# Kernel optimization log

Measured on AMD Instinct MI355X. Metric: run time of the kernel, lower is better.

## Reference

```python
import jax, jax.numpy as jnp
import numpy as np

D_MODEL = 1024
H = 16
D_K = D_MODEL // H


def setup_inputs() -> dict:
    key = jax.random.key(0)
    ks = jax.random.split(key, 12)
    B, S = 2, 2048
    q = jax.random.normal(ks[0], (B, S, D_MODEL), dtype=jnp.float32)
    k = jax.random.normal(ks[1], (B, S, D_MODEL), dtype=jnp.float32)
    v = jax.random.normal(ks[2], (B, S, D_MODEL), dtype=jnp.float32)
    mask = jax.random.randint(ks[3], (1, 1, S, S), 0, 2, dtype=jnp.int32)
    sc = 1.0 / np.sqrt(D_MODEL)
    wq = jax.random.uniform(ks[4], (D_MODEL, D_MODEL), jnp.float32, -sc, sc)
    bq = jax.random.uniform(ks[5], (D_MODEL,), jnp.float32, -sc, sc)
    wk = jax.random.uniform(ks[6], (D_MODEL, D_MODEL), jnp.float32, -sc, sc)
    bk = jax.random.uniform(ks[7], (D_MODEL,), jnp.float32, -sc, sc)
    wv = jax.random.uniform(ks[8], (D_MODEL, D_MODEL), jnp.float32, -sc, sc)
    bv = jax.random.uniform(ks[9], (D_MODEL,), jnp.float32, -sc, sc)
    wo = jax.random.uniform(ks[10], (D_MODEL, D_MODEL), jnp.float32, -sc, sc)
    bo = jax.random.uniform(ks[11], (D_MODEL,), jnp.float32, -sc, sc)
    return {"q": q, "k": k, "v": v, "mask": mask,
            "wq": wq, "bq": bq, "wk": wk, "bk": bk,
            "wv": wv, "bv": bv, "wo": wo, "bo": bo}


def reference(q, k, v, mask, wq, bq, wk, bk, wv, bv, wo, bo):
    B, S, _ = q.shape
    # linear projections (torch Linear: x @ W.T + b)
    query = q @ wq.T + bq
    key = k @ wk.T + bk
    value = v @ wv.T + bv
    # [B, S, D] -> [B, H, S, d_k]
    query = query.reshape(B, S, H, D_K).transpose(0, 2, 1, 3)
    key = key.reshape(B, S, H, D_K).transpose(0, 2, 1, 3)
    value = value.reshape(B, S, H, D_K).transpose(0, 2, 1, 3)
    scores = jnp.einsum('bhqd,bhkd->bhqk', query, key) / jnp.sqrt(
        jnp.asarray(D_K, query.dtype))
    # NOTE: source uses `-1 ** 9` which is -1 in Python, not -1e9 (soft mask)
    scores = jnp.where(mask == 0, jnp.asarray(-1.0, scores.dtype), scores)
    attn = jax.nn.softmax(scores, axis=-1)
    # source calls dropout(attn) but discards the result -> no-op
    x = jnp.einsum('bhqk,bhkd->bhqd', attn, value)
    x = x.transpose(0, 2, 1, 3).reshape(B, S, H * D_K)
    return x @ wo.T + bo
```

## Files before the change

kernel.cpp:

```cpp
#include <hip/hip_runtime.h>
#include <hip/hip_bf16.h>

#define D_MODEL 1024
#define NH 16
#define DK 64
#define S_LEN 2048
#define BATCH 2
#define M_ROWS (BATCH * S_LEN)

typedef float    floatx4 __attribute__((ext_vector_type(4)));
typedef _Float16 half8   __attribute__((ext_vector_type(8)));
typedef _Float16 half4v  __attribute__((ext_vector_type(4)));

#define LOG2E 1.4426950408889634f
#define EXPM1 0.36787944117144233f

__device__ __forceinline__ half8 ldh8(const _Float16* p) {
    return __builtin_bit_cast(half8, *(const uint4*)p);
}
__device__ __forceinline__ void gld16(const void* g, void* l) {
    __builtin_amdgcn_global_load_lds(
        (const __attribute__((address_space(1))) void*)g,
        (__attribute__((address_space(3))) void*)l, 16, 0, 0);
}
__device__ __forceinline__ float dpp_swap1(float x) {
    return __builtin_bit_cast(float,
        __builtin_amdgcn_mov_dpp(__builtin_bit_cast(int, x), 0xB1, 0xF, 0xF, false));
}

__global__ __launch_bounds__(256)
void cast_h(const float* __restrict__ s0, const float* __restrict__ s1,
            const float* __restrict__ s2, const float* __restrict__ s3,
            _Float16* __restrict__ out, int R) {
    const int z = blockIdx.y;
    const float* src = (z == 0) ? s0 : (z == 1) ? s1 : (z == 2) ? s2 : s3;
    const size_t idx = ((size_t)blockIdx.x * 256 + threadIdx.x) * 4;
    float4 v = *(const float4*)&src[idx];
    half4v h = {(_Float16)v.x, (_Float16)v.y, (_Float16)v.z, (_Float16)v.w};
    *(half4v*)&out[(size_t)z * R * 1024 + idx] = h;
}

template <int OUTMODE>
__global__ __launch_bounds__(256)
void gemm_f16(const _Float16* __restrict__ Abase, const _Float16* __restrict__ Wbase,
              const float* __restrict__ b0, const float* __restrict__ b1,
              const float* __restrict__ b2, void* __restrict__ Obase) {
    __shared__ __align__(16) _Float16 As[128 * 64];
    __shared__ __align__(16) _Float16 Ws[128 * 64];
    const int tid = threadIdx.x;
    const int w = tid >> 6, lane = tid & 63;
    const int l15 = lane & 15, q4 = lane >> 4;
    const int z = (OUTMODE == 1) ? blockIdx.z : 0;
    const int m0 = blockIdx.y * 128, n0 = blockIdx.x * 128;
    const int wm = w >> 1, wn = w & 1;

    const _Float16* A = Abase + (size_t)z * M_ROWS * 1024;
    const _Float16* W = Wbase + (size_t)z * 1024 * 1024;
    const float* bias = (OUTMODE == 1) ? ((z == 0) ? b0 : (z == 1) ? b1 : b2) : b0;

    int srow[4], sseg[4];
#pragma unroll
    for (int i = 0; i < 4; i++) {
        const int slot = i * 256 + tid;
        srow[i] = slot >> 3;
        sseg[i] = ((slot & 7) ^ (srow[i] & 7)) * 8;
    }

    int aoff[4][2], woff[4][2];
#pragma unroll
    for (int r = 0; r < 4; r++) {
        const int ar = wm * 64 + r * 16 + l15;
        const int wr = wn * 64 + r * 16 + l15;
#pragma unroll
        for (int kc = 0; kc < 2; kc++) {
            aoff[r][kc] = (ar * 8 + ((kc * 4 + q4) ^ (ar & 7))) * 8;
            woff[r][kc] = (wr * 8 + ((kc * 4 + q4) ^ (wr & 7))) * 8;
        }
    }

    floatx4 acc[4][4];
#pragma unroll
    for (int r = 0; r < 4; r++)
#pragma unroll
        for (int c = 0; c < 4; c++) acc[r][c] = (floatx4){0.f, 0.f, 0.f, 0.f};

    for (int k0 = 0; k0 < 1024; k0 += 64) {
#pragma unroll
        for (int i = 0; i < 4; i++) {
            const int lb = (i * 256 + w * 64) * 8;
            gld16(&A[(size_t)(m0 + srow[i]) * 1024 + k0 + sseg[i]], &As[lb]);
            gld16(&W[(size_t)(n0 + srow[i]) * 1024 + k0 + sseg[i]], &Ws[lb]);
        }
        __syncthreads();

        half8 af[4][2], wf[4][2];
#pragma unroll
        for (int r = 0; r < 4; r++)
#pragma unroll
            for (int kc = 0; kc < 2; kc++) {
                af[r][kc] = ldh8(&As[aoff[r][kc]]);
                wf[r][kc] = ldh8(&Ws[woff[r][kc]]);
            }
#pragma unroll
        for (int kc = 0; kc < 2; kc++)
#pragma unroll
            for (int r = 0; r < 4; r++)
#pragma unroll
                for (int c = 0; c < 4; c++)
                    acc[r][c] = __builtin_amdgcn_mfma_f32_16x16x32_f16(
                        af[r][kc], wf[c][kc], acc[r][c], 0, 0, 0);
        __syncthreads();
    }

#pragma unroll
    for (int r = 0; r < 4; r++)
#pragma unroll
        for (int c = 0; c < 4; c++)
#pragma unroll
            for (int reg = 0; reg < 4; reg++) {
                const int m = m0 + wm * 64 + r * 16 + q4 * 4 + reg;
                const int n = n0 + wn * 64 + c * 16 + l15;
                float val = acc[r][c][reg] + bias[n];
                if (OUTMODE == 0) {
                    ((float*)Obase)[(size_t)m * 1024 + n] = val;
                } else {
                    if (z == 0) val *= 0.125f * LOG2E;
                    const int b = m >> 11, s = m & 2047;
                    const int h = n >> 6, d = n & 63;
                    _Float16* Oz = (_Float16*)Obase + (size_t)z * M_ROWS * 1024;
                    Oz[(((size_t)(b * 16 + h) * S_LEN + s) << 6) + d] = (_Float16)val;
                }
            }
}

__global__ __launch_bounds__(256)
void vt_trans(const short* __restrict__ Vh, short* __restrict__ Vt) {
    __shared__ __align__(16) short T[64][80];
    const int bh = blockIdx.y;
    const int s0 = blockIdx.x * 64;
    const int t = threadIdx.x;
#pragma unroll
    for (int i = 0; i < 2; i++) {
        const int p = t + i * 256, r = p >> 3, c8 = (p & 7) * 8;
        uint4 raw = *(const uint4*)&Vh[((size_t)bh * S_LEN + s0 + r) * 64 + c8];
        const short* sv = (const short*)&raw;
#pragma unroll
        for (int j = 0; j < 8; j++) T[c8 + j][r] = sv[j];
    }
    __syncthreads();
#pragma unroll
    for (int i = 0; i < 2; i++) {
        const int p = t + i * 256, d = p >> 3, seg = (p & 7) * 8;
        *(uint4*)&Vt[((size_t)bh * DK + d) * S_LEN + s0 + seg] =
            *(const uint4*)&T[d][seg];
    }
}

__global__ __launch_bounds__(256)
void mask_pack(const int* __restrict__ mask, unsigned long long* __restrict__ mb) {
    const int gw = blockIdx.x * 4 + (threadIdx.x >> 6);
    const int lane = threadIdx.x & 63;
    const int row = gw >> 5, wid = gw & 31;
    const int mv = mask[(size_t)row * S_LEN + wid * 64 + lane];
    unsigned long long bal = __ballot(mv != 0);
    if (lane == 0) mb[gw] = bal;
}

__global__ __launch_bounds__(512, 4)
void attn_mfma(const _Float16* __restrict__ Qh, const _Float16* __restrict__ Kh,
               const _Float16* __restrict__ Vt, const unsigned long long* __restrict__ mb,
               _Float16* __restrict__ Xh) {
    __shared__ __align__(16) _Float16 Ks[2][64 * 64];
    __shared__ __align__(16) _Float16 Vs[2][64 * 64];
    __shared__ __align__(16) _Float16 Ps[8][32 * 72];

    const int tid = threadIdx.x;
    const int w = tid >> 6, lane = tid & 63;
    const int z = w >> 2, w4 = w & 3;
    const int t255 = tid & 255;
    const int l15 = lane & 15, q4 = lane >> 4;
    const int bh = blockIdx.y, b = bh >> 4, h = bh & 15;
    const int qb = blockIdx.x * 128 + w4 * 32;
    const int kbase = z * 1024;

    const _Float16* Qg = Qh + ((size_t)bh * S_LEN + qb) * DK;
    const _Float16* Kg = Kh + ((size_t)bh * S_LEN + kbase) * DK;
    const _Float16* Vg = Vt + (size_t)bh * DK * S_LEN + kbase;

    half8 Aq[2][2];
#pragma unroll
    for (int qs = 0; qs < 2; qs++)
#pragma unroll
        for (int ch = 0; ch < 2; ch++)
            Aq[qs][ch] = ldh8(&Qg[(qs * 16 + l15) * DK + ch * 32 + q4 * 8]);

    int grow[2], gseg[2];
#pragma unroll
    for (int i = 0; i < 2; i++) {
        const int slot = i * 256 + t255;
        grow[i] = slot >> 3;
        gseg[i] = ((slot & 7) ^ (grow[i] & 7)) * 8;
    }

    int kb[2];
#pragma unroll
    for (int ch = 0; ch < 2; ch++)
        kb[ch] = l15 * 64 + (((ch * 4 + q4) ^ (l15 & 7)) * 8);

    const unsigned long long* mrow_p = mb + (size_t)(qb + q4 * 4) * (S_LEN / 64) + z * 16;

    floatx4 O[2][4];
#pragma unroll
    for (int qs = 0; qs < 2; qs++)
#pragma unroll
        for (int nt = 0; nt < 4; nt++) O[qs][nt] = (floatx4){0.f, 0.f, 0.f, 0.f};
    floatx4 lacc[2];
    lacc[0] = (floatx4){0.f, 0.f, 0.f, 0.f};
    lacc[1] = (floatx4){0.f, 0.f, 0.f, 0.f};

    half8 onesB;
#pragma unroll
    for (int i = 0; i < 8; i++) onesB[i] = (_Float16)1.0f;

    const bool evenlane = ((lane & 1) == 0);

    for (int j0 = 0; j0 < 1024; j0 += 64) {
#pragma unroll
        for (int i = 0; i < 2; i++) {
            const int lb = (i * 256 + w4 * 64) * 8;
            gld16(&Kg[(size_t)(j0 + grow[i]) * DK + gseg[i]], &Ks[z][lb]);
            gld16(&Vg[(size_t)grow[i] * S_LEN + j0 + gseg[i]], &Vs[z][lb]);
        }
        const int jw = j0 >> 6;
        __syncthreads();

#pragma unroll
        for (int qs = 0; qs < 2; qs++) {
            unsigned long long mw[4];
#pragma unroll
            for (int reg = 0; reg < 4; reg++)
                mw[reg] = mrow_p[qs * 512 + reg * 32 + jw];

            floatx4 Sf[4];
#pragma unroll
            for (int jt = 0; jt < 4; jt++) {
                floatx4 c = (floatx4){0.f, 0.f, 0.f, 0.f};
                c = __builtin_amdgcn_mfma_f32_16x16x32_f16(
                    Aq[qs][0], ldh8(&Ks[z][jt * 1024 + kb[0]]), c, 0, 0, 0);
                c = __builtin_amdgcn_mfma_f32_16x16x32_f16(
                    Aq[qs][1], ldh8(&Ks[z][jt * 1024 + kb[1]]), c, 0, 0, 0);
                Sf[jt] = c;
            }
#pragma unroll
            for (int reg = 0; reg < 4; reg++) {
                const unsigned long long m = mw[reg];
                const unsigned tt0 = (unsigned)m >> l15;
                const unsigned tt1 = (unsigned)(m >> 32) >> l15;
#pragma unroll
                for (int jt = 0; jt < 4; jt++) {
                    float p = __builtin_amdgcn_exp2f(Sf[jt][reg]);
                    const unsigned sel = (jt < 2 ? tt0 : tt1) & (1u << ((jt & 1) * 16));
                    p = sel ? p : EXPM1;
                    const float po = dpp_swap1(p);
                    if (evenlane) {
                        *(unsigned*)&Ps[w][(qs * 16 + q4 * 4 + reg) * 72 +
                                           jt * 16 + l15] =
                            __builtin_bit_cast(unsigned,
                                __builtin_amdgcn_cvt_pkrtz(p, po));
                    }
                }
            }
        }

#pragma unroll
        for (int qs = 0; qs < 2; qs++) {
            half8 Ap[2];
#pragma unroll
            for (int ch = 0; ch < 2; ch++)
                Ap[ch] = ldh8(&Ps[w][(qs * 16 + l15) * 72 + ch * 32 + q4 * 8]);
            lacc[qs] = __builtin_amdgcn_mfma_f32_16x16x32_f16(Ap[0], onesB, lacc[qs], 0, 0, 0);
            lacc[qs] = __builtin_amdgcn_mfma_f32_16x16x32_f16(Ap[1], onesB, lacc[qs], 0, 0, 0);
#pragma unroll
            for (int nt = 0; nt < 4; nt++) {
                O[qs][nt] = __builtin_amdgcn_mfma_f32_16x16x32_f16(
                    Ap[0], ldh8(&Vs[z][nt * 1024 + kb[0]]), O[qs][nt], 0, 0, 0);
                O[qs][nt] = __builtin_amdgcn_mfma_f32_16x16x32_f16(
                    Ap[1], ldh8(&Vs[z][nt * 1024 + kb[1]]), O[qs][nt], 0, 0, 0);
            }
        }
        __syncthreads();
    }

    float* Obuf = (float*)&Ps[0][0];
    if (z == 1) {
#pragma unroll
        for (int qs = 0; qs < 2; qs++)
#pragma unroll
            for (int reg = 0; reg < 4; reg++) {
                const int rl = w4 * 32 + qs * 16 + q4 * 4 + reg;
#pragma unroll
                for (int nt = 0; nt < 4; nt++)
                    Obuf[rl * 65 + nt * 16 + l15] = O[qs][nt][reg];
                if (l15 == 0) Obuf[rl * 65 + 64] = lacc[qs][reg];
            }
    }
    __syncthreads();
    if (z == 0) {
#pragma unroll
        for (int qs = 0; qs < 2; qs++)
#pragma unroll
            for (int reg = 0; reg < 4; reg++) {
                const int rl = w4 * 32 + qs * 16 + q4 * 4 + reg;
                const float inv = 1.0f / (lacc[qs][reg] + Obuf[rl * 65 + 64]);
                const int srow = qb + qs * 16 + q4 * 4 + reg;
                _Float16* Xrow = Xh + (size_t)(b * S_LEN + srow) * 1024 + h * DK;
#pragma unroll
                for (int nt = 0; nt < 4; nt++)
                    Xrow[nt * 16 + l15] =
                        (_Float16)((O[qs][nt][reg] + Obuf[rl * 65 + nt * 16 + l15]) * inv);
            }
    }
}

extern "C" void kernel_launch(void* const* d_in, const int* in_sizes, int n_in,
                              void* d_out, int out_size, void* d_ws, size_t ws_size,
                              hipStream_t stream) {
    const float* q  = (const float*)d_in[0];
    const float* k  = (const float*)d_in[1];
    const float* v  = (const float*)d_in[2];
    const int* mask = (const int*)d_in[3];
    const float* wq = (const float*)d_in[4];
    const float* bq = (const float*)d_in[5];
    const float* wk = (const float*)d_in[6];
    const float* bk = (const float*)d_in[7];
    const float* wv = (const float*)d_in[8];
    const float* bv = (const float*)d_in[9];
    const float* wo = (const float*)d_in[10];
    const float* bo = (const float*)d_in[11];
    float* out = (float*)d_out;

    char* ws = (char*)d_ws;
    const size_t MB = 1u << 20;
    _Float16* Wh   = (_Float16*)ws;
    _Float16* Ah   = (_Float16*)(ws + 8 * MB);
    _Float16* QKVh = (_Float16*)(ws + 32 * MB);
    _Float16* Vt   = (_Float16*)(ws + 56 * MB);
    unsigned long long* mb = (unsigned long long*)(ws + 64 * MB);
    _Float16* Xh   = Ah;

    cast_h<<<dim3(1024, 4), 256, 0, stream>>>(wq, wk, wv, wo, Wh, 1024);
    cast_h<<<dim3(4096, 3), 256, 0, stream>>>(q, k, v, nullptr, Ah, M_ROWS);

    gemm_f16<1><<<dim3(8, 32, 3), 256, 0, stream>>>(Ah, Wh, bq, bk, bv, QKVh);

    vt_trans<<<dim3(32, 32), 256, 0, stream>>>(
        (const short*)(QKVh + (size_t)2 * M_ROWS * 1024), (short*)Vt);
    mask_pack<<<S_LEN * (S_LEN / 64) / 4, 256, 0, stream>>>(mask, mb);

    attn_mfma<<<dim3(16, 32), 512, 0, stream>>>(QKVh, QKVh + (size_t)M_ROWS * 1024,
                                                Vt, mb, Xh);

    gemm_f16<0><<<dim3(8, 32, 1), 256, 0, stream>>>(Xh, Wh + (size_t)3 * 1024 * 1024,
                                                    bo, bo, bo, out);
}
```

Before: 285.8 us.

## Fuse V transpose into QKV GEMM epilogue and software-pipeline K/V loads in attention

The QKV projection GEMM now writes V directly in transposed [b,h,d,s] layout, which removes the separate vt_trans kernel launch and its read/write pass over V. In the attention kernel, K and V tile loads for the next iteration are issued right after the current tile is consumed. Explicit vmcnt waits and raw barriers replace the full __syncthreads, so the loads overlap with the QK and PV MFMA phases. Mask word loads are interleaved with the score MFMAs. The manual waitcnt and barrier choreography is fragile, and the loop issues one extra prefetch that wraps to index 0 on its last iteration.

```diff
diff --git a/kernel.cpp b/kernel.cpp
--- a/kernel.cpp
+++ b/kernel.cpp
@@ -26,6 +26,11 @@
 __device__ __forceinline__ float dpp_swap1(float x) {
     return __builtin_bit_cast(float,
         __builtin_amdgcn_mov_dpp(__builtin_bit_cast(int, x), 0xB1, 0xF, 0xF, false));
+}
+__device__ __forceinline__ void rawbar() {
+    __builtin_amdgcn_sched_barrier(0);
+    __builtin_amdgcn_s_barrier();
+    __builtin_amdgcn_sched_barrier(0);
 }
 
 __global__ __launch_bounds__(256)
@@ -44,7 +49,8 @@
 __global__ __launch_bounds__(256)
 void gemm_f16(const _Float16* __restrict__ Abase, const _Float16* __restrict__ Wbase,
               const float* __restrict__ b0, const float* __restrict__ b1,
-              const float* __restrict__ b2, void* __restrict__ Obase) {
+              const float* __restrict__ b2, void* __restrict__ Obase,
+              void* __restrict__ Obase2) {
     __shared__ __align__(16) _Float16 As[128 * 64];
     __shared__ __align__(16) _Float16 Ws[128 * 64];
     const int tid = threadIdx.x;
@@ -115,15 +121,29 @@
 #pragma unroll
     for (int r = 0; r < 4; r++)
 #pragma unroll
-        for (int c = 0; c < 4; c++)
-#pragma unroll
-            for (int reg = 0; reg < 4; reg++) {
-                const int m = m0 + wm * 64 + r * 16 + q4 * 4 + reg;
-                const int n = n0 + wn * 64 + c * 16 + l15;
-                float val = acc[r][c][reg] + bias[n];
-                if (OUTMODE == 0) {
-                    ((float*)Obase)[(size_t)m * 1024 + n] = val;
-                } else {
+        for (int c = 0; c < 4; c++) {
+            const int n = n0 + wn * 64 + c * 16 + l15;
+            const int mbase = m0 + wm * 64 + r * 16 + q4 * 4;
+            float vals[4];
+#pragma unroll
+            for (int reg = 0; reg < 4; reg++) vals[reg] = acc[r][c][reg] + bias[n];
+
+            if (OUTMODE == 0) {
+#pragma unroll
+                for (int reg = 0; reg < 4; reg++)
+                    ((float*)Obase)[(size_t)(mbase + reg) * 1024 + n] = vals[reg];
+            } else if (z == 2) {
+                const int b = mbase >> 11, s = mbase & 2047;
+                const int h = n >> 6, d = n & 63;
+                half4v hv = {(_Float16)vals[0], (_Float16)vals[1],
+                             (_Float16)vals[2], (_Float16)vals[3]};
+                *(half4v*)&((_Float16*)Obase2)[
+                    (((size_t)((b * 16 + h) * 64 + d)) << 11) + s] = hv;
+            } else {
+#pragma unroll
+                for (int reg = 0; reg < 4; reg++) {
+                    const int m = mbase + reg;
+                    float val = vals[reg];
                     if (z == 0) val *= 0.125f * LOG2E;
                     const int b = m >> 11, s = m & 2047;
                     const int h = n >> 6, d = n & 63;
@@ -131,29 +151,7 @@
                     Oz[(((size_t)(b * 16 + h) * S_LEN + s) << 6) + d] = (_Float16)val;
                 }
             }
-}
-
-__global__ __launch_bounds__(256)
-void vt_trans(const short* __restrict__ Vh, short* __restrict__ Vt) {
-    __shared__ __align__(16) short T[64][80];
-    const int bh = blockIdx.y;
-    const int s0 = blockIdx.x * 64;
-    const int t = threadIdx.x;
-#pragma unroll
-    for (int i = 0; i < 2; i++) {
-        const int p = t + i * 256, r = p >> 3, c8 = (p & 7) * 8;
-        uint4 raw = *(const uint4*)&Vh[((size_t)bh * S_LEN + s0 + r) * 64 + c8];
-        const short* sv = (const short*)&raw;
-#pragma unroll
-        for (int j = 0; j < 8; j++) T[c8 + j][r] = sv[j];
-    }
-    __syncthreads();
-#pragma unroll
-    for (int i = 0; i < 2; i++) {
-        const int p = t + i * 256, d = p >> 3, seg = (p & 7) * 8;
-        *(uint4*)&Vt[((size_t)bh * DK + d) * S_LEN + s0 + seg] =
-            *(const uint4*)&T[d][seg];
-    }
+        }
 }
 
 __global__ __launch_bounds__(256)
@@ -224,24 +222,28 @@
 
     const bool evenlane = ((lane & 1) == 0);
 
+#pragma unroll
+    for (int i = 0; i < 2; i++) {
+        const int lb = (i * 256 + w4 * 64) * 8;
+        gld16(&Kg[(size_t)grow[i] * DK + gseg[i]], &Ks[z][lb]);
+    }
+#pragma unroll
+    for (int i = 0; i < 2; i++) {
+        const int lb = (i * 256 + w4 * 64) * 8;
+        gld16(&Vg[(size_t)grow[i] * S_LEN + gseg[i]], &Vs[z][lb]);
+    }
+
     for (int j0 = 0; j0 < 1024; j0 += 64) {
-#pragma unroll
-        for (int i = 0; i < 2; i++) {
-            const int lb = (i * 256 + w4 * 64) * 8;
-            gld16(&Kg[(size_t)(j0 + grow[i]) * DK + gseg[i]], &Ks[z][lb]);
-            gld16(&Vg[(size_t)grow[i] * S_LEN + j0 + gseg[i]], &Vs[z][lb]);
-        }
+        const int jn = (j0 + 64) & 1023;
         const int jw = j0 >> 6;
-        __syncthreads();
+
+        __builtin_amdgcn_sched_barrier(0);
+        asm volatile("s_waitcnt vmcnt(2)" ::: "memory");
+        rawbar();
 
 #pragma unroll
         for (int qs = 0; qs < 2; qs++) {
             unsigned long long mw[4];
-#pragma unroll
-            for (int reg = 0; reg < 4; reg++)
-                mw[reg] = mrow_p[qs * 512 + reg * 32 + jw];
-
-            floatx4 Sf[4];
 #pragma unroll
             for (int jt = 0; jt < 4; jt++) {
                 floatx4 c = (floatx4){0.f, 0.f, 0.f, 0.f};
@@ -249,17 +251,17 @@
                     Aq[qs][0], ldh8(&Ks[z][jt * 1024 + kb[0]]), c, 0, 0, 0);
                 c = __builtin_amdgcn_mfma_f32_16x16x32_f16(
                     Aq[qs][1], ldh8(&Ks[z][jt * 1024 + kb[1]]), c, 0, 0, 0);
-                Sf[jt] = c;
-            }
-#pragma unroll
-            for (int reg = 0; reg < 4; reg++) {
-                const unsigned long long m = mw[reg];
-                const unsigned tt0 = (unsigned)m >> l15;
-                const unsigned tt1 = (unsigned)(m >> 32) >> l15;
-#pragma unroll
-                for (int jt = 0; jt < 4; jt++) {
-                    float p = __builtin_amdgcn_exp2f(Sf[jt][reg]);
-                    const unsigned sel = (jt < 2 ? tt0 : tt1) & (1u << ((jt & 1) * 16));
+                if (jt == 0) {
+#pragma unroll
+                    for (int reg = 0; reg < 4; reg++)
+                        mw[reg] = mrow_p[qs * 512 + reg * 32 + jw];
+                }
+#pragma unroll
+                for (int reg = 0; reg < 4; reg++) {
+                    const unsigned ttw =
+                        (unsigned)(mw[reg] >> (jt >= 2 ? 32 : 0)) >> l15;
+                    const unsigned sel = ttw & (1u << ((jt & 1) * 16));
+                    float p = __builtin_amdgcn_exp2f(c[reg]);
                     p = sel ? p : EXPM1;
                     const float po = dpp_swap1(p);
                     if (evenlane) {
@@ -272,6 +274,17 @@
             }
         }
 
+        rawbar();
+#pragma unroll
+        for (int i = 0; i < 2; i++) {
+            const int lb = (i * 256 + w4 * 64) * 8;
+            gld16(&Kg[(size_t)(jn + grow[i]) * DK + gseg[i]], &Ks[z][lb]);
+        }
+
+        __builtin_amdgcn_sched_barrier(0);
+        asm volatile("s_waitcnt vmcnt(2)" ::: "memory");
+        rawbar();
+
 #pragma unroll
         for (int qs = 0; qs < 2; qs++) {
             half8 Ap[2];
@@ -288,8 +301,15 @@
                     Ap[1], ldh8(&Vs[z][nt * 1024 + kb[1]]), O[qs][nt], 0, 0, 0);
             }
         }
-        __syncthreads();
-    }
+
+        rawbar();
+#pragma unroll
+        for (int i = 0; i < 2; i++) {
+            const int lb = (i * 256 + w4 * 64) * 8;
+            gld16(&Vg[(size_t)grow[i] * S_LEN + jn + gseg[i]], &Vs[z][lb]);
+        }
+    }
+    __builtin_amdgcn_sched_barrier(0);
 
     float* Obuf = (float*)&Ps[0][0];
     if (z == 1) {
@@ -351,15 +371,13 @@
     cast_h<<<dim3(1024, 4), 256, 0, stream>>>(wq, wk, wv, wo, Wh, 1024);
     cast_h<<<dim3(4096, 3), 256, 0, stream>>>(q, k, v, nullptr, Ah, M_ROWS);
 
-    gemm_f16<1><<<dim3(8, 32, 3), 256, 0, stream>>>(Ah, Wh, bq, bk, bv, QKVh);
-
-    vt_trans<<<dim3(32, 32), 256, 0, stream>>>(
-        (const short*)(QKVh + (size_t)2 * M_ROWS * 1024), (short*)Vt);
+    gemm_f16<1><<<dim3(8, 32, 3), 256, 0, stream>>>(Ah, Wh, bq, bk, bv, QKVh, Vt);
+
     mask_pack<<<S_LEN * (S_LEN / 64) / 4, 256, 0, stream>>>(mask, mb);
 
     attn_mfma<<<dim3(16, 32), 512, 0, stream>>>(QKVh, QKVh + (size_t)M_ROWS * 1024,
                                                 Vt, mb, Xh);
 
     gemm_f16<0><<<dim3(8, 32, 1), 256, 0, stream>>>(Xh, Wh + (size_t)3 * 1024 * 1024,
-                                                    bo, bo, bo, out);
-}
+                                                    bo, bo, bo, out, nullptr);
+}
```

Result: no change. 284.9 us (-0.3%).
